# Performance work log

Hardware: AMD Instinct MI355X
Metric: run time of the kernel (lower is better)

Reference implementation:

```python
import jax, jax.numpy as jnp
import numpy as np

# GCN over dependency trees (aryehgigi/gcn-over-pruned-trees), eval mode:
# dropout = identity, rnn=False, dep_dim=0, no_adj=False.
# Per layer l: Ax = adj @ x ; AxW = Linear_l(Ax) + Linear_l(x) (bias counted twice,
# faithful to `self.W[l](Ax) + self.W[l](gcn_inputs)`) ; AxW /= (adj.sum(2)+1) ; relu.

B, L = 128, 256
VOCAB, EMB, POSV, POSD, NERV, NERD, MEM = 50000, 300, 52, 30, 20, 30, 200
IN_DIM = EMB + POSD + NERD  # 360


def setup_inputs() -> dict:
    key = jax.random.key(0)
    ks = jax.random.split(key, 11)
    words = jax.random.randint(ks[0], (B, L), 0, VOCAB)
    pos = jax.random.randint(ks[1], (B, L), 0, POSV)
    ner = jax.random.randint(ks[2], (B, L), 0, NERV)
    adj = (jax.random.uniform(ks[3], (B, L, L)) < 0.05).astype(jnp.float32)
    emb_W = jax.random.normal(ks[4], (VOCAB, EMB), jnp.float32) * 0.1
    pos_W = jax.random.normal(ks[5], (POSV, POSD), jnp.float32) * 0.1
    ner_W = jax.random.normal(ks[6], (NERV, NERD), jnp.float32) * 0.1
    W0 = jax.random.normal(ks[7], (MEM, IN_DIM), jnp.float32) * (1.0 / np.sqrt(IN_DIM))
    b0 = jnp.zeros((MEM,), jnp.float32)
    W1 = jax.random.normal(ks[8], (MEM, MEM), jnp.float32) * (1.0 / np.sqrt(MEM))
    b1 = jnp.zeros((MEM,), jnp.float32)
    return {"words": words, "pos": pos, "ner": ner, "adj": adj,
            "emb_W": emb_W, "pos_W": pos_W, "ner_W": ner_W,
            "W0": W0, "b0": b0, "W1": W1, "b1": b1}


def reference(words, pos, ner, adj, emb_W, pos_W, ner_W, W0, b0, W1, b1):
    # embedding lookups + concat -> [B, L, IN_DIM]
    x = jnp.concatenate([emb_W[words], pos_W[pos], ner_W[ner]], axis=2)
    denom = jnp.sum(adj, axis=2, keepdims=True) + 1.0  # [B, L, 1]
    mask = ((jnp.sum(adj, axis=2) + jnp.sum(adj, axis=1)) == 0)[..., None]  # [B, L, 1]
    for W, b in ((W0, b0), (W1, b1)):
        Ax = jnp.einsum('bij,bjd->bid', adj, x)  # message passing
        # W(Ax) + W(x) == (Ax + x) @ W.T + 2*b  (bias applied twice, as in source)
        h = (jnp.einsum('bld,md->blm', Ax + x, W) + 2.0 * b) / denom
        x = jax.nn.relu(h)
    return (x, mask)
```

## Files before the change

### kernel.cpp

```cpp
#include <hip/hip_runtime.h>
#include <hip/hip_bf16.h>
#include <stdint.h>

typedef __attribute__((ext_vector_type(8))) short short8;
typedef __attribute__((ext_vector_type(4))) float f32x4;

#define NB 128
#define NL 256
#define NROWS 32768
#define IN_DIM 360
#define KP1 384
#define MEM 200
#define NP 256
#define OUT_X (NROWS * MEM)
#define YTP 264
#define BUFSZ 20480
#define YTOFF 40960


__device__ __forceinline__ unsigned short f2b(float f) {
    unsigned u = __builtin_bit_cast(unsigned, f);
    unsigned r = (u + 0x7FFFu + ((u >> 16) & 1u)) >> 16;
    return (unsigned short)r;
}

__device__ __forceinline__ short8 gather_chunk(int chunk, const float* __restrict__ er,
                                               const float* __restrict__ pr,
                                               const float* __restrict__ nr) {
    float v[8];
    if (chunk < 37) {
        const float* s = er + chunk * 8;
        float4 a = *(const float4*)s;
        float4 b = *(const float4*)(s + 4);
        v[0] = a.x; v[1] = a.y; v[2] = a.z; v[3] = a.w;
        v[4] = b.x; v[5] = b.y; v[6] = b.z; v[7] = b.w;
    } else if (chunk == 37) {
        float4 a = *(const float4*)(er + 296);
        v[0] = a.x; v[1] = a.y; v[2] = a.z; v[3] = a.w;
        v[4] = 0.f; v[5] = 0.f; v[6] = 0.f; v[7] = 0.f;
    } else if (chunk <= 41) {
        int k0 = chunk * 8 - 304;
        #pragma unroll
        for (int i = 0; i < 8; ++i) v[i] = (k0 + i < 30) ? pr[k0 + i] : 0.f;
    } else if (chunk <= 45) {
        int k0 = chunk * 8 - 336;
        #pragma unroll
        for (int i = 0; i < 8; ++i) v[i] = (k0 + i < 30) ? nr[k0 + i] : 0.f;
    } else {
        #pragma unroll
        for (int i = 0; i < 8; ++i) v[i] = 0.f;
    }
    short8 r;
    #pragma unroll
    for (int i = 0; i < 8; ++i) r[i] = (short)f2b(v[i]);
    return r;
}

__global__ void prep_weights(const float* __restrict__ W0, const float* __restrict__ W1,
                             short* __restrict__ W0p, short* __restrict__ W1p,
                             unsigned* __restrict__ colnz) {
    int idx = blockIdx.x * 256 + threadIdx.x;
    if (idx < NROWS) colnz[idx] = 0u;
    if (idx < NP * KP1) {
        int n = idx / KP1, kp = idx - n * KP1;
        float v = 0.f;
        if (n < MEM) {
            if (kp < 300)                   v = W0[n * IN_DIM + kp];
            else if (kp >= 304 && kp < 334) v = W0[n * IN_DIM + 300 + (kp - 304)];
            else if (kp >= 336 && kp < 366) v = W0[n * IN_DIM + 330 + (kp - 336)];
        }
        W0p[idx] = (short)f2b(v);
    } else {
        int i2 = idx - NP * KP1;
        if (i2 < NP * NP) {
            int n = i2 >> 8, k = i2 & 255;
            float v = (n < MEM && k < MEM) ? W1[n * MEM + k] : 0.f;
            W1p[i2] = (short)f2b(v);
        }
    }
}

__global__ void adjrow_kernel(const float* __restrict__ adj, float* __restrict__ dinv,
                              float* __restrict__ rsum, unsigned short* __restrict__ Sbf,
                              unsigned* __restrict__ colnz) {
    int row = blockIdx.x * 4 + (threadIdx.x >> 6);
    int lane = threadIdx.x & 63;
    const float4* ar = (const float4*)(adj + (size_t)row * NL);
    float4 v = ar[lane];
    float s = v.x + v.y + v.z + v.w;
    #pragma unroll
    for (int off = 32; off >= 1; off >>= 1) s += __shfl_xor(s, off);
    int rloc = row & 255;
    float d0 = v.x + ((lane * 4 + 0) == rloc ? 1.f : 0.f);
    float d1 = v.y + ((lane * 4 + 1) == rloc ? 1.f : 0.f);
    float d2 = v.z + ((lane * 4 + 2) == rloc ? 1.f : 0.f);
    float d3 = v.w + ((lane * 4 + 3) == rloc ? 1.f : 0.f);
    ushort4 st; st.x = f2b(d0); st.y = f2b(d1); st.z = f2b(d2); st.w = f2b(d3);
    *(ushort4*)(Sbf + (size_t)row * NL + lane * 4) = st;
    if (lane == 0) { rsum[row] = s; dinv[row] = 1.0f / (s + 1.0f); }
    unsigned* cz = colnz + ((row >> 8) << 8);
    if (v.x != 0.f) atomicOr(&cz[lane * 4 + 0], 1u);
    if (v.y != 0.f) atomicOr(&cz[lane * 4 + 1], 1u);
    if (v.z != 0.f) atomicOr(&cz[lane * 4 + 2], 1u);
    if (v.w != 0.f) atomicOr(&cz[lane * 4 + 3], 1u);
}

template <int FINAL>
__global__ __launch_bounds__(512, 4) void fused_kernel(
    const short* __restrict__ A, int lda, int nkt,
    const short* __restrict__ Bp, int ldb,
    const unsigned short* __restrict__ Sbf,
    const float* __restrict__ dinv, const float* __restrict__ bias,
    const int* __restrict__ words, const int* __restrict__ pos, const int* __restrict__ ner,
    const float* __restrict__ embW, const float* __restrict__ posW,
    const float* __restrict__ nerW,
    const float* __restrict__ rsum, const unsigned* __restrict__ colnz,
    float* __restrict__ maskout,
    short* __restrict__ x1b, float* __restrict__ outx) {
    extern __shared__ char smem[];
    unsigned short* Yt = (unsigned short*)(smem + YTOFF);

    int bi = blockIdx.x;
    int batch = bi & 127, sl = bi >> 7;

    int tid = threadIdx.x;
    int lane = tid & 63, wid = tid >> 6;
    int wr = wid >> 1, wc = wid & 1;
    int lr = lane & 15, lc = lane >> 4;

    if (FINAL == 0 && sl == 0 && tid < 256) {
        int r = batch * NL + tid;
        maskout[r] = (rsum[r] == 0.f && colnz[r] == 0u) ? 1.0f : 0.0f;
    }

    const short* Bb = Bp + (size_t)sl * 64 * ldb;
    const short* Sb = (const short*)(Sbf + (size_t)batch * NL * NL);

    int r0s = tid >> 2, c0s = tid & 3;
    int r1s = r0s + 128;
    int offA0 = r0s * 64 + (c0s ^ ((r0s >> 1) & 3)) * 16;
    int offA1 = r1s * 64 + (c0s ^ ((r1s >> 1) & 3)) * 16;
    const short* Sp0 = Sb + (size_t)r0s * NL + c0s * 8;
    const short* Sp1 = Sb + (size_t)r1s * NL + c0s * 8;
    int offB = 0; const short* Bpp = nullptr;
    if (tid < 256) {
        int br = tid >> 2, bc = tid & 3;
        offB = 16384 + br * 64 + (bc ^ ((br >> 1) & 3)) * 16;
        Bpp = Bb + (size_t)br * ldb + bc * 8;
    }

    const short* Ap0 = nullptr; const short* Ap1 = nullptr;
    const float *er0 = nullptr, *pr0 = nullptr, *nr0 = nullptr;
    const float *er1 = nullptr, *pr1 = nullptr, *nr1 = nullptr;
    if (FINAL == 0) {
        int g0 = batch * NL + r0s, g1 = g0 + 128;
        er0 = embW + (size_t)words[g0] * 300;
        pr0 = posW + (size_t)pos[g0] * 30;
        nr0 = nerW + (size_t)ner[g0] * 30;
        er1 = embW + (size_t)words[g1] * 300;
        pr1 = posW + (size_t)pos[g1] * 30;
        nr1 = nerW + (size_t)ner[g1] * 30;
    } else {
        const short* Ab = A + (size_t)batch * NL * lda;
        Ap0 = Ab + (size_t)r0s * lda + c0s * 8;
        Ap1 = Ab + (size_t)r1s * lda + c0s * 8;
    }
    #define LOADA(kt, o0, o1) do {                                  \
        if (FINAL == 0) {                                           \
            int ch_ = (kt) * 4 + c0s;                               \
            (o0) = gather_chunk(ch_, er0, pr0, nr0);                \
            (o1) = gather_chunk(ch_, er1, pr1, nr1);                \
        } else {                                                    \
            (o0) = *(const short8*)(Ap0 + (kt) * 32);               \
            (o1) = *(const short8*)(Ap1 + (kt) * 32);               \
        }                                                           \
    } while (0)

    f32x4 acc[4][2] = {};
    short8 aR0, aR1, bR;
    LOADA(0, aR0, aR1);
    if (tid < 256) bR = *(const short8*)Bpp;
    *(short8*)(smem + offA0) = aR0;
    *(short8*)(smem + offA1) = aR1;
    if (tid < 256) *(short8*)(smem + offB) = bR;
    LOADA(1, aR0, aR1);
    if (tid < 256) bR = *(const short8*)(Bpp + 32);
    __syncthreads();

    short8 sA0, sA1, sB0, sB1;
    for (int kt = 0; kt < nkt; ++kt) {
        char* base_ = smem + (kt & 1) * BUFSZ;
        short8 af[4], bf[2];
        #pragma unroll
        for (int mi = 0; mi < 4; ++mi) {
            int row = wr * 64 + mi * 16 + lr;
            int cs = lc ^ ((row >> 1) & 3);
            af[mi] = *(const short8*)(base_ + row * 64 + cs * 16);
        }
        #pragma unroll
        for (int ni = 0; ni < 2; ++ni) {
            int row = wc * 32 + ni * 16 + lr;
            int cs = lc ^ ((row >> 1) & 3);
            bf[ni] = *(const short8*)(base_ + 16384 + row * 64 + cs * 16);
        }
        if (kt + 1 < nkt) {
            char* nb_ = smem + ((kt + 1) & 1) * BUFSZ;
            *(short8*)(nb_ + offA0) = aR0;
            *(short8*)(nb_ + offA1) = aR1;
            if (tid < 256) *(short8*)(nb_ + offB) = bR;
        }
        if (kt + 2 < nkt) {
            LOADA(kt + 2, aR0, aR1);
            if (tid < 256) bR = *(const short8*)(Bpp + (kt + 2) * 32);
        } else if (kt + 2 == nkt) {
            sA0 = *(const short8*)Sp0;
            sA1 = *(const short8*)Sp1;
        } else if (kt + 2 == nkt + 1) {
            sB0 = *(const short8*)(Sp0 + 32);
            sB1 = *(const short8*)(Sp1 + 32);
        }
        #pragma unroll
        for (int mi = 0; mi < 4; ++mi)
            #pragma unroll
            for (int ni = 0; ni < 2; ++ni)
                acc[mi][ni] = __builtin_amdgcn_mfma_f32_16x16x32_bf16(af[mi], bf[ni], acc[mi][ni], 0, 0, 0);
        __syncthreads();
    }
    #undef LOADA

    #pragma unroll
    for (int mi = 0; mi < 4; ++mi)
        #pragma unroll
        for (int ni = 0; ni < 2; ++ni) {
            f32x4 v = acc[mi][ni];
            ushort4 st; st.x = f2b(v[0]); st.y = f2b(v[1]); st.z = f2b(v[2]); st.w = f2b(v[3]);
            int col = wc * 32 + ni * 16 + lr;
            int row0 = wr * 64 + mi * 16 + lc * 4;
            *(ushort4*)(Yt + (size_t)col * YTP + row0) = st;
        }
    *(short8*)(smem + offA0) = sA0;
    *(short8*)(smem + offA1) = sA1;
    sA0 = *(const short8*)(Sp0 + 64);
    sA1 = *(const short8*)(Sp1 + 64);
    __syncthreads();

    f32x4 acc2[4][2] = {};
    #pragma unroll
    for (int kt = 0; kt < 8; ++kt) {
        char* base_ = smem + (kt & 1) * BUFSZ;
        short8 ay[4], bs[2];
        #pragma unroll
        for (int mi = 0; mi < 4; ++mi)
            ay[mi] = *(const short8*)(Yt + (size_t)(mi * 16 + lr) * YTP + kt * 32 + lc * 8);
        #pragma unroll
        for (int ni = 0; ni < 2; ++ni) {
            int row = wid * 32 + ni * 16 + lr;
            int cs = lc ^ ((row >> 1) & 3);
            bs[ni] = *(const short8*)(base_ + row * 64 + cs * 16);
        }
        if (kt + 1 < 8) {
            char* nb_ = smem + ((kt + 1) & 1) * BUFSZ;
            if ((kt & 1) == 0) {
                *(short8*)(nb_ + offA0) = sB0;
                *(short8*)(nb_ + offA1) = sB1;
                if (kt + 3 < 8) {
                    sB0 = *(const short8*)(Sp0 + (kt + 3) * 32);
                    sB1 = *(const short8*)(Sp1 + (kt + 3) * 32);
                }
            } else {
                *(short8*)(nb_ + offA0) = sA0;
                *(short8*)(nb_ + offA1) = sA1;
                if (kt + 3 < 8) {
                    sA0 = *(const short8*)(Sp0 + (kt + 3) * 32);
                    sA1 = *(const short8*)(Sp1 + (kt + 3) * 32);
                }
            }
        }
        #pragma unroll
        for (int mi = 0; mi < 4; ++mi)
            #pragma unroll
            for (int ni = 0; ni < 2; ++ni)
                acc2[mi][ni] = __builtin_amdgcn_mfma_f32_16x16x32_bf16(ay[mi], bs[ni], acc2[mi][ni], 0, 0, 0);
        if (kt + 1 < 8) __syncthreads();
    }

    #pragma unroll
    for (int ni = 0; ni < 2; ++ni) {
        int g = batch * NL + wid * 32 + ni * 16 + lr;
        float di = dinv[g];
        #pragma unroll
        for (int mi = 0; mi < 4; ++mi) {
            int col0 = sl * 64 + mi * 16 + lc * 4;
            float4 bv;
            if (col0 < MEM) bv = *(const float4*)(bias + col0);
            else { bv.x = 0.f; bv.y = 0.f; bv.z = 0.f; bv.w = 0.f; }
            f32x4 z = acc2[mi][ni];
            float h0 = fmaxf((z[0] + 2.f * bv.x) * di, 0.f);
            float h1 = fmaxf((z[1] + 2.f * bv.y) * di, 0.f);
            float h2 = fmaxf((z[2] + 2.f * bv.z) * di, 0.f);
            float h3 = fmaxf((z[3] + 2.f * bv.w) * di, 0.f);
            if (FINAL == 0) {
                ushort4 st; st.x = f2b(h0); st.y = f2b(h1); st.z = f2b(h2); st.w = f2b(h3);
                *(ushort4*)((unsigned short*)x1b + (size_t)g * NP + col0) = st;
            } else if (col0 < MEM) {
                float4 o; o.x = h0; o.y = h1; o.z = h2; o.w = h3;
                *(float4*)(outx + (size_t)g * MEM + col0) = o;
            }
        }
    }
}

extern "C" void kernel_launch(void* const* d_in, const int* in_sizes, int n_in,
                              void* d_out, int out_size, void* d_ws, size_t ws_size,
                              hipStream_t stream) {
    const int*   words = (const int*)d_in[0];
    const int*   pos   = (const int*)d_in[1];
    const int*   ner   = (const int*)d_in[2];
    const float* adj   = (const float*)d_in[3];
    const float* embW  = (const float*)d_in[4];
    const float* posW  = (const float*)d_in[5];
    const float* nerW  = (const float*)d_in[6];
    const float* W0    = (const float*)d_in[7];
    const float* b0    = (const float*)d_in[8];
    const float* W1    = (const float*)d_in[9];
    const float* b1    = (const float*)d_in[10];
    float* out = (float*)d_out;

    char* ws = (char*)d_ws;
    size_t off = 0;
    short* W0p = (short*)(ws + off);        off += (size_t)NP * KP1 * 2;
    short* W1p = (short*)(ws + off);        off += (size_t)NP * NP * 2;
    short* X1b = (short*)(ws + off);        off += (size_t)NROWS * NP * 2;
    float* dinv = (float*)(ws + off);       off += (size_t)NROWS * 4;
    float* rsum = (float*)(ws + off);       off += (size_t)NROWS * 4;
    unsigned* colnz = (unsigned*)(ws + off); off += (size_t)NROWS * 4;
    unsigned short* Sbf = (unsigned short*)(ws + off); off += (size_t)NROWS * NL * 2;

    prep_weights<<<(NP * KP1 + NP * NP + 255) / 256, 256, 0, stream>>>(W0, W1, W0p, W1p, colnz);
    adjrow_kernel<<<NROWS / 4, 256, 0, stream>>>(adj, dinv, rsum, Sbf, colnz);

    const int ldsB = YTOFF + 64 * YTP * 2;
    fused_kernel<0><<<NB * 4, 512, ldsB, stream>>>(nullptr, KP1, KP1 / 32, W0p, KP1,
                                                   Sbf, dinv, b0,
                                                   words, pos, ner, embW, posW, nerW,
                                                   rsum, colnz, out + OUT_X,
                                                   X1b, nullptr);
    fused_kernel<1><<<NB * 4, 512, ldsB, stream>>>(X1b, NP, NP / 32, W1p, NP,
                                                   Sbf, dinv, b1,
                                                   nullptr, nullptr, nullptr, nullptr, nullptr, nullptr,
                                                   nullptr, nullptr, nullptr,
                                                   nullptr, out);
}
```

Measured before the change: 81.96 us.

## Add dedicated layer-1 kernel using direct global-to-LDS async loads

```diff
diff --git a/kernel.cpp b/kernel.cpp
--- a/kernel.cpp
+++ b/kernel.cpp
@@ -22,6 +22,11 @@
     unsigned u = __builtin_bit_cast(unsigned, f);
     unsigned r = (u + 0x7FFFu + ((u >> 16) & 1u)) >> 16;
     return (unsigned short)r;
+}
+
+__device__ __forceinline__ void gl16(const void* g, void* l) {
+    __builtin_amdgcn_global_load_lds((const __attribute__((address_space(1))) unsigned*)g,
+                                     (__attribute__((address_space(3))) unsigned*)l, 16, 0, 0);
 }
 
 __device__ __forceinline__ short8 gather_chunk(int chunk, const float* __restrict__ er,
@@ -149,10 +154,9 @@
         Bpp = Bb + (size_t)br * ldb + bc * 8;
     }
 
-    const short* Ap0 = nullptr; const short* Ap1 = nullptr;
     const float *er0 = nullptr, *pr0 = nullptr, *nr0 = nullptr;
     const float *er1 = nullptr, *pr1 = nullptr, *nr1 = nullptr;
-    if (FINAL == 0) {
+    {
         int g0 = batch * NL + r0s, g1 = g0 + 128;
         er0 = embW + (size_t)words[g0] * 300;
         pr0 = posW + (size_t)pos[g0] * 30;
@@ -160,20 +164,11 @@
         er1 = embW + (size_t)words[g1] * 300;
         pr1 = posW + (size_t)pos[g1] * 30;
         nr1 = nerW + (size_t)ner[g1] * 30;
-    } else {
-        const short* Ab = A + (size_t)batch * NL * lda;
-        Ap0 = Ab + (size_t)r0s * lda + c0s * 8;
-        Ap1 = Ab + (size_t)r1s * lda + c0s * 8;
     }
     #define LOADA(kt, o0, o1) do {                                  \
-        if (FINAL == 0) {                                           \
-            int ch_ = (kt) * 4 + c0s;                               \
-            (o0) = gather_chunk(ch_, er0, pr0, nr0);                \
-            (o1) = gather_chunk(ch_, er1, pr1, nr1);                \
-        } else {                                                    \
-            (o0) = *(const short8*)(Ap0 + (kt) * 32);               \
-            (o1) = *(const short8*)(Ap1 + (kt) * 32);               \
-        }                                                           \
+        int ch_ = (kt) * 4 + c0s;                                   \
+        (o0) = gather_chunk(ch_, er0, pr0, nr0);                    \
+        (o1) = gather_chunk(ch_, er1, pr1, nr1);                    \
     } while (0)
 
     f32x4 acc[4][2] = {};
@@ -299,11 +294,149 @@
             float h1 = fmaxf((z[1] + 2.f * bv.y) * di, 0.f);
             float h2 = fmaxf((z[2] + 2.f * bv.z) * di, 0.f);
             float h3 = fmaxf((z[3] + 2.f * bv.w) * di, 0.f);
-            if (FINAL == 0) {
-                ushort4 st; st.x = f2b(h0); st.y = f2b(h1); st.z = f2b(h2); st.w = f2b(h3);
-                *(ushort4*)((unsigned short*)x1b + (size_t)g * NP + col0) = st;
-            } else if (col0 < MEM) {
-                float4 o; o.x = h0; o.y = h1; o.z = h2; o.w = h3;
+            ushort4 st; st.x = f2b(h0); st.y = f2b(h1); st.z = f2b(h2); st.w = f2b(h3);
+            *(ushort4*)((unsigned short*)x1b + (size_t)g * NP + col0) = st;
+        }
+    }
+}
+
+__global__ __launch_bounds__(512, 4) void fused1_kernel(
+    const short* __restrict__ A,
+    const short* __restrict__ Bp,
+    const unsigned short* __restrict__ Sbf,
+    const float* __restrict__ dinv, const float* __restrict__ bias,
+    float* __restrict__ outx) {
+    extern __shared__ char smem[];
+    unsigned short* Yt = (unsigned short*)(smem + YTOFF);
+
+    int bi = blockIdx.x;
+    int batch = bi & 127, sl = bi >> 7;
+    int tid = threadIdx.x;
+    int lane = tid & 63, wid = tid >> 6;
+    int wr = wid >> 1, wc = wid & 1;
+    int lr = lane & 15, lc = lane >> 4;
+
+    const short* Ab = A + (size_t)batch * NL * NP;
+    const short* Bb = Bp + (size_t)sl * 64 * NP;
+    const short* Sb = (const short*)(Sbf + (size_t)batch * NL * NL);
+
+    int li0 = tid, li1 = tid + 512;
+    int rA0 = li0 >> 2, cA0 = (li0 & 3) ^ ((rA0 >> 1) & 3);
+    int rA1 = li1 >> 2, cA1 = (li1 & 3) ^ ((rA1 >> 1) & 3);
+    const short* srcA0 = Ab + (size_t)rA0 * NP + cA0 * 8;
+    const short* srcA1 = Ab + (size_t)rA1 * NP + cA1 * 8;
+    const short* srcS0 = Sb + (size_t)rA0 * NL + cA0 * 8;
+    const short* srcS1 = Sb + (size_t)rA1 * NL + cA1 * 8;
+    const short* srcB = nullptr;
+    if (wid < 4) {
+        int rB = tid >> 2, cB = (tid & 3) ^ ((rB >> 1) & 3);
+        srcB = Bb + (size_t)rB * NP + cB * 8;
+    }
+    int dA0 = (wid * 64) * 16;
+    int dA1 = (512 + wid * 64) * 16;
+    int dB  = 16384 + (wid * 64) * 16;
+
+    #define STAGE1(b, kt) do {                                       \
+        char* bb_ = smem + (b) * BUFSZ;                              \
+        gl16(srcA0 + (kt) * 32, bb_ + dA0);                          \
+        gl16(srcA1 + (kt) * 32, bb_ + dA1);                          \
+        if (wid < 4) gl16(srcB + (kt) * 32, bb_ + dB);               \
+    } while (0)
+    #define STAGES(b, kt) do {                                       \
+        char* bb_ = smem + (b) * BUFSZ;                              \
+        gl16(srcS0 + (kt) * 32, bb_ + dA0);                          \
+        gl16(srcS1 + (kt) * 32, bb_ + dA1);                         \
+    } while (0)
+    #define WAITBAR() do {                                           \
+        asm volatile("s_waitcnt vmcnt(0)" ::: "memory");             \
+        __builtin_amdgcn_sched_barrier(0);                           \
+        __builtin_amdgcn_s_barrier();                                \
+    } while (0)
+
+    f32x4 acc[4][2] = {};
+    STAGE1(0, 0);
+    WAITBAR();
+    #pragma unroll
+    for (int kt = 0; kt < 8; ++kt) {
+        if (kt + 1 < 8) STAGE1((kt + 1) & 1, kt + 1);
+        char* base_ = smem + (kt & 1) * BUFSZ;
+        short8 af[4], bf[2];
+        #pragma unroll
+        for (int mi = 0; mi < 4; ++mi) {
+            int row = wr * 64 + mi * 16 + lr;
+            int cs = lc ^ ((row >> 1) & 3);
+            af[mi] = *(const short8*)(base_ + row * 64 + cs * 16);
+        }
+        #pragma unroll
+        for (int ni = 0; ni < 2; ++ni) {
+            int row = wc * 32 + ni * 16 + lr;
+            int cs = lc ^ ((row >> 1) & 3);
+            bf[ni] = *(const short8*)(base_ + 16384 + row * 64 + cs * 16);
+        }
+        #pragma unroll
+        for (int mi = 0; mi < 4; ++mi)
+            #pragma unroll
+            for (int ni = 0; ni < 2; ++ni)
+                acc[mi][ni] = __builtin_amdgcn_mfma_f32_16x16x32_bf16(af[mi], bf[ni], acc[mi][ni], 0, 0, 0);
+        WAITBAR();
+    }
+
+    STAGES(0, 0);
+    #pragma unroll
+    for (int mi = 0; mi < 4; ++mi)
+        #pragma unroll
+        for (int ni = 0; ni < 2; ++ni) {
+            f32x4 v = acc[mi][ni];
+            ushort4 st; st.x = f2b(v[0]); st.y = f2b(v[1]); st.z = f2b(v[2]); st.w = f2b(v[3]);
+            int col = wc * 32 + ni * 16 + lr;
+            int row0 = wr * 64 + mi * 16 + lc * 4;
+            *(ushort4*)(Yt + (size_t)col * YTP + row0) = st;
+        }
+    asm volatile("s_waitcnt vmcnt(0)" ::: "memory");
+    __builtin_amdgcn_sched_barrier(0);
+    __syncthreads();
+
+    f32x4 acc2[4][2] = {};
+    #pragma unroll
+    for (int kt = 0; kt < 8; ++kt) {
+        if (kt + 1 < 8) STAGES((kt + 1) & 1, kt + 1);
+        char* base_ = smem + (kt & 1) * BUFSZ;
+        short8 ay[4], bs[2];
+        #pragma unroll
+        for (int mi = 0; mi < 4; ++mi)
+            ay[mi] = *(const short8*)(Yt + (size_t)(mi * 16 + lr) * YTP + kt * 32 + lc * 8);
+        #pragma unroll
+        for (int ni = 0; ni < 2; ++ni) {
+            int row = wid * 32 + ni * 16 + lr;
+            int cs = lc ^ ((row >> 1) & 3);
+            bs[ni] = *(const short8*)(base_ + row * 64 + cs * 16);
+        }
+        #pragma unroll
+        for (int mi = 0; mi < 4; ++mi)
+            #pragma unroll
+            for (int ni = 0; ni < 2; ++ni)
+                acc2[mi][ni] = __builtin_amdgcn_mfma_f32_16x16x32_bf16(ay[mi], bs[ni], acc2[mi][ni], 0, 0, 0);
+        if (kt + 1 < 8) WAITBAR();
+    }
+    #undef STAGE1
+    #undef STAGES
+    #undef WAITBAR
+
+    #pragma unroll
+    for (int ni = 0; ni < 2; ++ni) {
+        int g = batch * NL + wid * 32 + ni * 16 + lr;
+        float di = dinv[g];
+        #pragma unroll
+        for (int mi = 0; mi < 4; ++mi) {
+            int col0 = sl * 64 + mi * 16 + lc * 4;
+            if (col0 < MEM) {
+                float4 bv = *(const float4*)(bias + col0);
+                f32x4 z = acc2[mi][ni];
+                float4 o;
+                o.x = fmaxf((z[0] + 2.f * bv.x) * di, 0.f);
+                o.y = fmaxf((z[1] + 2.f * bv.y) * di, 0.f);
+                o.z = fmaxf((z[2] + 2.f * bv.z) * di, 0.f);
+                o.w = fmaxf((z[3] + 2.f * bv.w) * di, 0.f);
                 *(float4*)(outx + (size_t)g * MEM + col0) = o;
             }
         }
@@ -345,9 +478,5 @@
                                                    words, pos, ner, embW, posW, nerW,
                                                    rsum, colnz, out + OUT_X,
                                                    X1b, nullptr);
-    fused_kernel<1><<<NB * 4, 512, ldsB, stream>>>(X1b, NP, NP / 32, W1p, NP,
-                                                   Sbf, dinv, b1,
-                                                   nullptr, nullptr, nullptr, nullptr, nullptr, nullptr,
-                                                   nullptr, nullptr, nullptr,
-                                                   nullptr, out);
-}
+    fused1_kernel<<<NB * 4, 512, ldsB, stream>>>(X1b, W1p, Sbf, dinv, b1, out);
+}
```

After: 81.29 us. Within noise of the previous version (-0.8%).
